# Performance work log

Hardware: AMD Instinct MI355X
Metric: run time of the kernel (lower is better)

## Reference

```python
import jax, jax.numpy as jnp
import numpy as np

N_NODES = 100000
N_EDGES = 1000000
F_IN = 128
HID = 128
OUT = 64


def setup_inputs() -> dict:
    key = jax.random.key(0)
    ks = jax.random.split(key, 8)
    node_features = jax.random.normal(ks[0], (N_NODES, F_IN), dtype=jnp.float32)
    edge_index = jax.random.randint(ks[1], (2, N_EDGES), 0, N_NODES, dtype=jnp.int64)
    s1 = 1.0 / np.sqrt(F_IN)
    s2 = 1.0 / np.sqrt(HID)
    W1 = jax.random.uniform(ks[2], (F_IN, HID), jnp.float32, -s1, s1)
    b1 = jax.random.uniform(ks[3], (HID,), jnp.float32, -s1, s1)
    W2 = jax.random.uniform(ks[4], (HID, HID), jnp.float32, -s2, s2)
    b2 = jax.random.uniform(ks[5], (HID,), jnp.float32, -s2, s2)
    Wp = jax.random.uniform(ks[6], (HID, OUT), jnp.float32, -s2, s2)
    bp = jax.random.uniform(ks[7], (OUT,), jnp.float32, -s2, s2)
    return {"node_features": node_features, "edge_index": edge_index,
            "W1": W1, "b1": b1, "W2": W2, "b2": b2, "Wp": Wp, "bp": bp}


def reference(node_features, edge_index, W1, b1, W2, b2, Wp, bp):
    # encoder: Linear -> ReLU -> Linear
    h = jax.nn.relu(node_features @ W1 + b1) @ W2 + b2  # [N, HID]
    src = edge_index[0]
    dst = edge_index[1]
    # per-edge gather of h[src], scatter-add into dst (segment reduce)
    messages = jax.ops.segment_sum(h[src], dst, num_segments=h.shape[0])  # [N, HID]
    h = h + messages
    pooled = jnp.mean(h, axis=0)  # [HID]
    return pooled @ Wp + bp  # [OUT]
```

## Files before the change

### kernel.cpp

```cpp
#include <hip/hip_runtime.h>
#include <hip/hip_bf16.h>
#include <stdint.h>

typedef __attribute__((ext_vector_type(8))) short short8;
typedef __attribute__((ext_vector_type(4))) float f32x4;
typedef __attribute__((ext_vector_type(4))) int i32x4;

#define RANGE  51200
#define RWORDS 25600
#define NSL    32
#define NFRAG  16

static __device__ __forceinline__ short to_bf16s(float f) {
  __hip_bfloat16 h = __float2bfloat16(f);
  return __builtin_bit_cast(short, h);
}

__global__ __launch_bounds__(1024) void k_histprep(
    const int* __restrict__ e, unsigned* __restrict__ priv,
    short* __restrict__ frag, const float* __restrict__ W1, int E) {
  __shared__ unsigned cnt[RWORDS];
  __shared__ int is64s;
  int b = blockIdx.x, tid = threadIdx.x;
  if (b < NFRAG) {
    int idx = b * 1024 + tid;
    int k = idx >> 7, col = idx & 127;
    int ct = col >> 4, ks = k >> 5, lh = (k >> 3) & 3, ee = k & 7;
    int lane = lh * 16 + (col & 15);
    frag[((ct * 4 + ks) * 64 + lane) * 8 + ee] = to_bf16s(W1[idx]);
    return;
  }
  int h = b - NFRAG;
  int r = h >> 5, s = h & (NSL - 1);
  if (tid < 64) {
    unsigned long long bl = __ballot(e[2 * tid + 1] == 0);
    if (tid == 0) is64s = (__popcll(bl) > 32) ? 1 : 0;
  }
  for (int j = tid; j < RWORDS; j += 1024) cnt[j] = 0u;
  __syncthreads();
  int is64 = is64s;
  unsigned base = (unsigned)r * RANGE;
  int nq = E >> 2;
  int qlo = (int)((long long)s * nq / NSL);
  int qhi = (int)((long long)(s + 1) * nq / NSL);
  for (int q = qlo + tid; q < qhi; q += 1024) {
    i32x4 v;
    if (is64) {
      i32x4 a = *reinterpret_cast<const i32x4*>(e + 8 * (size_t)q);
      i32x4 bb = *reinterpret_cast<const i32x4*>(e + 8 * (size_t)q + 4);
      v = i32x4{a[0], a[2], bb[0], bb[2]};
    } else {
      v = *reinterpret_cast<const i32x4*>(e + 4 * (size_t)q);
    }
#pragma unroll
    for (int k = 0; k < 4; ++k) {
      unsigned loc = (unsigned)v[k] - base;
      if (loc < (unsigned)RANGE)
        atomicAdd(&cnt[loc >> 1], 1u << (16 * (loc & 1)));
    }
  }
  if (s == 0) {
    int tail = E & 3;
    if (tid < tail) {
      int idx = E - tail + tid;
      unsigned loc = (unsigned)(is64 ? e[2 * idx] : e[idx]) - base;
      if (loc < (unsigned)RANGE)
        atomicAdd(&cnt[loc >> 1], 1u << (16 * (loc & 1)));
    }
  }
  __syncthreads();
  unsigned* dst = priv + (size_t)h * RWORDS;
  for (int j = tid; j < RWORDS; j += 1024) dst[j] = cnt[j];
}

__global__ __launch_bounds__(256) void k_main(
    const float* __restrict__ X, const short* __restrict__ w1frag,
    const float* __restrict__ b1, const unsigned* __restrict__ priv,
    const float* __restrict__ wdegG, float* __restrict__ partials,
    int nNodes) {
  __shared__ __align__(16) short w1s[16384];
  __shared__ __align__(16) short xs[8192];
  __shared__ __align__(16) float scratch[320];

  int tid = threadIdx.x;
  {
    const f32x4* src = reinterpret_cast<const f32x4*>(w1frag);
    f32x4* dst = reinterpret_cast<f32x4*>(w1s);
#pragma unroll
    for (int i = 0; i < 8; ++i) dst[tid + i * 256] = src[tid + i * 256];
  }
  unsigned* degacc = (unsigned*)scratch;
  float* wdeg_s = scratch + 256;

  int lane = tid & 63, wave = tid >> 6;
  int rA = lane & 15;
  int kh = lane >> 4;

  float b1r[8];
#pragma unroll
  for (int ct = 0; ct < 8; ++ct) b1r[ct] = b1[ct * 16 + rA];

  float sl[8] = {0, 0, 0, 0, 0, 0, 0, 0};
  int nChunks = (nNodes + 63) >> 6;
  __syncthreads();

  for (int c = blockIdx.x; c < nChunks; c += gridDim.x) {
    int row0 = c << 6;
#pragma unroll
    for (int p = 0; p < 4; ++p) {
      int j = p * 256 + tid;
      int rl = j >> 4, kc = j & 15;
      int grow = row0 + rl;
      if (grow > nNodes - 1) grow = nNodes - 1;
      const f32x4* gp =
          reinterpret_cast<const f32x4*>(X + (size_t)grow * 128 + kc * 8);
      f32x4 lo = gp[0], hi = gp[1];
      short8 v;
#pragma unroll
      for (int ee = 0; ee < 4; ++ee) {
        v[ee] = to_bf16s(lo[ee]);
        v[4 + ee] = to_bf16s(hi[ee]);
      }
      int u = rl * 16 + (kc ^ (rl & 7));
      *reinterpret_cast<short8*>(&xs[u * 8]) = v;
    }
    if (wdegG) {
      if (tid < 64) {
        int row = row0 + tid;
        wdeg_s[tid] = (row < nNodes) ? wdegG[row] : 0.f;
      }
    } else {
      int r = row0 / RANGE;
      int w0 = (row0 - r * RANGE) >> 1;
      int j = tid & 31, sg = tid >> 5;
      const unsigned* pp =
          priv + ((size_t)(r * NSL + sg * 4)) * RWORDS + w0 + j;
      unsigned ssum = 0;
#pragma unroll
      for (int q = 0; q < 4; ++q) ssum += pp[(size_t)q * RWORDS];
      degacc[sg * 32 + j] = ssum;
    }
    __syncthreads();
    if (!wdegG && tid < 32) {
      unsigned wsum = 0;
#pragma unroll
      for (int g = 0; g < 8; ++g) wsum += degacc[g * 32 + tid];
      wdeg_s[2 * tid] = 1.0f + (float)(wsum & 0xFFFFu);
      wdeg_s[2 * tid + 1] = 1.0f + (float)(wsum >> 16);
    }
    int rloc = wave * 16 + rA;
    f32x4 acc[8];
#pragma unroll
    for (int ct = 0; ct < 8; ++ct) acc[ct] = f32x4{0.f, 0.f, 0.f, 0.f};
#pragma unroll
    for (int ks = 0; ks < 4; ++ks) {
      int kc = ks * 4 + kh;
      int u = rloc * 16 + (kc ^ (rloc & 7));
      short8 a = *reinterpret_cast<const short8*>(&xs[u * 8]);
#pragma unroll
      for (int ct = 0; ct < 8; ++ct) {
        short8 bfr = *reinterpret_cast<const short8*>(
            &w1s[((ct * 4 + ks) * 64 + lane) * 8]);
        acc[ct] = __builtin_amdgcn_mfma_f32_16x16x32_bf16(a, bfr, acc[ct], 0, 0, 0);
      }
    }
    __syncthreads();
#pragma unroll
    for (int rr = 0; rr < 4; ++rr) {
      int rl = wave * 16 + kh * 4 + rr;
      float w = (row0 + rl < nNodes) ? wdeg_s[rl] : 0.0f;
#pragma unroll
      for (int ct = 0; ct < 8; ++ct)
        sl[ct] += w * fmaxf(acc[ct][rr] + b1r[ct], 0.f);
    }
    __syncthreads();
  }

  if (tid < 128) scratch[tid] = 0.f;
  __syncthreads();
#pragma unroll
  for (int ct = 0; ct < 8; ++ct) {
    float v = sl[ct];
    v += __shfl_xor(v, 16);
    v += __shfl_xor(v, 32);
    if (kh == 0) atomicAdd(&scratch[ct * 16 + rA], v);
  }
  __syncthreads();
  if (tid < 128) partials[(size_t)blockIdx.x * 128 + tid] = scratch[tid];
}

__global__ __launch_bounds__(1024) void k_final(
    const float* __restrict__ partials, int B, const float* __restrict__ W2,
    const float* __restrict__ b2, const float* __restrict__ Wp,
    const float* __restrict__ bp, float* __restrict__ out,
    float totalW, float invN) {
  __shared__ float accsA[32 * 128];
  __shared__ float sv[128];
  __shared__ float pooled[128];
  int t = threadIdx.x;
  {
    int cg = t & 31, slc = t >> 5;
    f32x4 s = f32x4{0.f, 0.f, 0.f, 0.f};
    for (int r = slc; r < B; r += 32)
      s += *reinterpret_cast<const f32x4*>(partials + (size_t)r * 128 + cg * 4);
    *reinterpret_cast<f32x4*>(&accsA[slc * 128 + cg * 4]) = s;
  }
  __syncthreads();
  if (t < 128) {
    float v = 0.f;
#pragma unroll
    for (int i = 0; i < 32; ++i) v += accsA[i * 128 + t];
    sv[t] = v;
  }
  __syncthreads();
  {
    int col = t & 127, sl8 = t >> 7;
    float a = 0.f;
#pragma unroll
    for (int kk = 0; kk < 16; ++kk) {
      int k = sl8 * 16 + kk;
      a += sv[k] * W2[k * 128 + col];
    }
    accsA[sl8 * 128 + col] = a;
  }
  __syncthreads();
  if (t < 128) {
    float v = totalW * b2[t];
#pragma unroll
    for (int i = 0; i < 8; ++i) v += accsA[i * 128 + t];
    pooled[t] = v * invN;
  }
  __syncthreads();
  if (t < 512) {
    int o = t & 63, s2 = t >> 6;
    float a = 0.f;
#pragma unroll
    for (int kk = 0; kk < 16; ++kk) {
      int k = s2 * 16 + kk;
      a += pooled[k] * Wp[k * 64 + o];
    }
    accsA[s2 * 64 + o] = a;
  }
  __syncthreads();
  if (t < 64) {
    float v = bp[t];
#pragma unroll
    for (int i = 0; i < 8; ++i) v += accsA[i * 64 + t];
    out[t] = v;
  }
}

__global__ void k_zero(unsigned* __restrict__ p, int n) {
  int i = blockIdx.x * 256 + threadIdx.x;
  if (i < n) p[i] = 0u;
}
__global__ __launch_bounds__(256) void k_hist_fb(const int* __restrict__ e,
                                                 unsigned* __restrict__ deg,
                                                 int E) {
  __shared__ int is64s;
  int tid = threadIdx.x;
  if (tid < 64) {
    unsigned long long bl = __ballot(e[2 * tid + 1] == 0);
    if (tid == 0) is64s = (__popcll(bl) > 32) ? 1 : 0;
  }
  __syncthreads();
  int is64 = is64s;
  int stride = gridDim.x * blockDim.x;
  for (int i = blockIdx.x * blockDim.x + tid; i < E; i += stride)
    atomicAdd(&deg[is64 ? (unsigned)e[2 * i] : (unsigned)e[i]], 1u);
}
__global__ void k_cvt(const unsigned* __restrict__ deg,
                      float* __restrict__ wdeg, int N) {
  int i = blockIdx.x * 256 + threadIdx.x;
  if (i < N) wdeg[i] = 1.0f + (float)deg[i];
}

extern "C" void kernel_launch(void* const* d_in, const int* in_sizes, int n_in,
                              void* d_out, int out_size, void* d_ws, size_t ws_size,
                              hipStream_t stream) {
  const float* X  = (const float*)d_in[0];
  const int*   ei = (const int*)d_in[1];
  const float* W1 = (const float*)d_in[2];
  const float* b1 = (const float*)d_in[3];
  const float* W2 = (const float*)d_in[4];
  const float* b2 = (const float*)d_in[5];
  const float* Wp = (const float*)d_in[6];
  const float* bp = (const float*)d_in[7];

  int N = in_sizes[0] / 128;
  int E = in_sizes[1] / 2;
  int nChunks = (N + 63) >> 6;
  int mb = nChunks < 521 ? nChunks : 521;

  size_t privB = (size_t)2 * NSL * RWORDS * 4;
  size_t fragB = (16384 * 2 + 255) & ~(size_t)255;
  size_t wdegB = ((size_t)N * 4 + 255) & ~(size_t)255;
  size_t partB = ((size_t)mb * 128 * 4 + 255) & ~(size_t)255;
  size_t fixed = privB + fragB + wdegB + partB + 512;

  bool fast = (N <= 2 * RANGE) && (E / NSL <= 60000) && (ws_size >= fixed);

  char* p = (char*)d_ws;
  unsigned* priv = (unsigned*)p;  p += privB;
  short* frag = (short*)p;        p += fragB;
  float* wdeg = (float*)p;        p += wdegB;
  float* parts = (float*)p;

  if (fast) {
    k_histprep<<<NFRAG + 2 * NSL, 1024, 0, stream>>>(ei, priv, frag, W1, E);
    k_main<<<mb, 256, 0, stream>>>(X, frag, b1, priv, (const float*)nullptr,
                                   parts, N);
  } else {
    k_histprep<<<NFRAG, 1024, 0, stream>>>(ei, priv, frag, W1, E);
    k_zero<<<(N + 255) / 256, 256, 0, stream>>>((unsigned*)wdeg, N);
    k_hist_fb<<<2048, 256, 0, stream>>>(ei, (unsigned*)wdeg, E);
    k_cvt<<<(N + 255) / 256, 256, 0, stream>>>((unsigned*)wdeg, wdeg, N);
    k_main<<<mb, 256, 0, stream>>>(X, frag, b1, priv, wdeg, parts, N);
  }
  k_final<<<1, 1024, 0, stream>>>(parts, mb, W2, b2, Wp, bp, (float*)d_out,
                                  (float)N + (float)E, 1.0f / (float)N);
}
```

Measured before the change: 39.15 us.

## Split degree merge into own kernel and make main loop per-wave without LDS staging

```diff
diff --git a/kernel.cpp b/kernel.cpp
--- a/kernel.cpp
+++ b/kernel.cpp
@@ -4,11 +4,12 @@
 
 typedef __attribute__((ext_vector_type(8))) short short8;
 typedef __attribute__((ext_vector_type(4))) float f32x4;
+typedef __attribute__((ext_vector_type(2))) float f32x2;
 typedef __attribute__((ext_vector_type(4))) int i32x4;
 
 #define RANGE  51200
 #define RWORDS 25600
-#define NSL    32
+#define NSL    64
 #define NFRAG  16
 
 static __device__ __forceinline__ short to_bf16s(float f) {
@@ -31,7 +32,7 @@
     return;
   }
   int h = b - NFRAG;
-  int r = h >> 5, s = h & (NSL - 1);
+  int r = h & 1, s = h >> 1;
   if (tid < 64) {
     unsigned long long bl = __ballot(e[2 * tid + 1] == 0);
     if (tid == 0) is64s = (__popcll(bl) > 32) ? 1 : 0;
@@ -73,14 +74,35 @@
   for (int j = tid; j < RWORDS; j += 1024) dst[j] = cnt[j];
 }
 
+__global__ __launch_bounds__(256) void k_merge(const unsigned* __restrict__ priv,
+                                               float* __restrict__ wdeg, int N) {
+  int g = blockIdx.x * 256 + threadIdx.x;
+  if (g >= 2 * RWORDS) return;
+  int r = (g >= RWORDS) ? 1 : 0;
+  int word = g - r * RWORDS;
+  const unsigned* p = priv + (size_t)r * RWORDS + word;
+  unsigned lo = 0, hi = 0;
+#pragma unroll 8
+  for (int s = 0; s < NSL; ++s) {
+    unsigned v = p[(size_t)(2 * s) * RWORDS];
+    lo += v & 0xFFFFu;
+    hi += v >> 16;
+  }
+  int n0 = r * RANGE + 2 * word;
+  if (n0 + 1 < N) {
+    *reinterpret_cast<f32x2*>(wdeg + n0) =
+        f32x2{1.0f + (float)lo, 1.0f + (float)hi};
+  } else if (n0 < N) {
+    wdeg[n0] = 1.0f + (float)lo;
+  }
+}
+
 __global__ __launch_bounds__(256) void k_main(
     const float* __restrict__ X, const short* __restrict__ w1frag,
-    const float* __restrict__ b1, const unsigned* __restrict__ priv,
-    const float* __restrict__ wdegG, float* __restrict__ partials,
-    int nNodes) {
+    const float* __restrict__ b1, const float* __restrict__ wdeg,
+    float* __restrict__ partials, int nNodes) {
   __shared__ __align__(16) short w1s[16384];
-  __shared__ __align__(16) short xs[8192];
-  __shared__ __align__(16) float scratch[320];
+  __shared__ float sred[128];
 
   int tid = threadIdx.x;
   {
@@ -89,8 +111,7 @@
 #pragma unroll
     for (int i = 0; i < 8; ++i) dst[tid + i * 256] = src[tid + i * 256];
   }
-  unsigned* degacc = (unsigned*)scratch;
-  float* wdeg_s = scratch + 256;
+  if (tid < 128) sred[tid] = 0.f;
 
   int lane = tid & 63, wave = tid >> 6;
   int rA = lane & 15;
@@ -101,62 +122,31 @@
   for (int ct = 0; ct < 8; ++ct) b1r[ct] = b1[ct * 16 + rA];
 
   float sl[8] = {0, 0, 0, 0, 0, 0, 0, 0};
-  int nChunks = (nNodes + 63) >> 6;
-  __syncthreads();
-
-  for (int c = blockIdx.x; c < nChunks; c += gridDim.x) {
-    int row0 = c << 6;
-#pragma unroll
-    for (int p = 0; p < 4; ++p) {
-      int j = p * 256 + tid;
-      int rl = j >> 4, kc = j & 15;
-      int grow = row0 + rl;
-      if (grow > nNodes - 1) grow = nNodes - 1;
-      const f32x4* gp =
-          reinterpret_cast<const f32x4*>(X + (size_t)grow * 128 + kc * 8);
-      f32x4 lo = gp[0], hi = gp[1];
-      short8 v;
+  int nChunks = (nNodes + 15) >> 4;
+  int gw = blockIdx.x * 4 + wave;
+  int nw = gridDim.x * 4;
+  __syncthreads();
+
+  for (int c = gw; c < nChunks; c += nw) {
+    int row0 = c << 4;
+    int rowA = row0 + rA;
+    if (rowA > nNodes - 1) rowA = nNodes - 1;
+    const float* xp = X + (size_t)rowA * 128 + kh * 8;
+
+    f32x4 acc[8];
+#pragma unroll
+    for (int ct = 0; ct < 8; ++ct) acc[ct] = f32x4{0.f, 0.f, 0.f, 0.f};
+
+#pragma unroll
+    for (int ks = 0; ks < 4; ++ks) {
+      f32x4 lo = *reinterpret_cast<const f32x4*>(xp + ks * 32);
+      f32x4 hi = *reinterpret_cast<const f32x4*>(xp + ks * 32 + 4);
+      short8 a;
 #pragma unroll
       for (int ee = 0; ee < 4; ++ee) {
-        v[ee] = to_bf16s(lo[ee]);
-        v[4 + ee] = to_bf16s(hi[ee]);
+        a[ee] = to_bf16s(lo[ee]);
+        a[4 + ee] = to_bf16s(hi[ee]);
       }
-      int u = rl * 16 + (kc ^ (rl & 7));
-      *reinterpret_cast<short8*>(&xs[u * 8]) = v;
-    }
-    if (wdegG) {
-      if (tid < 64) {
-        int row = row0 + tid;
-        wdeg_s[tid] = (row < nNodes) ? wdegG[row] : 0.f;
-      }
-    } else {
-      int r = row0 / RANGE;
-      int w0 = (row0 - r * RANGE) >> 1;
-      int j = tid & 31, sg = tid >> 5;
-      const unsigned* pp =
-          priv + ((size_t)(r * NSL + sg * 4)) * RWORDS + w0 + j;
-      unsigned ssum = 0;
-#pragma unroll
-      for (int q = 0; q < 4; ++q) ssum += pp[(size_t)q * RWORDS];
-      degacc[sg * 32 + j] = ssum;
-    }
-    __syncthreads();
-    if (!wdegG && tid < 32) {
-      unsigned wsum = 0;
-#pragma unroll
-      for (int g = 0; g < 8; ++g) wsum += degacc[g * 32 + tid];
-      wdeg_s[2 * tid] = 1.0f + (float)(wsum & 0xFFFFu);
-      wdeg_s[2 * tid + 1] = 1.0f + (float)(wsum >> 16);
-    }
-    int rloc = wave * 16 + rA;
-    f32x4 acc[8];
-#pragma unroll
-    for (int ct = 0; ct < 8; ++ct) acc[ct] = f32x4{0.f, 0.f, 0.f, 0.f};
-#pragma unroll
-    for (int ks = 0; ks < 4; ++ks) {
-      int kc = ks * 4 + kh;
-      int u = rloc * 16 + (kc ^ (rloc & 7));
-      short8 a = *reinterpret_cast<const short8*>(&xs[u * 8]);
 #pragma unroll
       for (int ct = 0; ct < 8; ++ct) {
         short8 bfr = *reinterpret_cast<const short8*>(
@@ -164,29 +154,26 @@
         acc[ct] = __builtin_amdgcn_mfma_f32_16x16x32_bf16(a, bfr, acc[ct], 0, 0, 0);
       }
     }
-    __syncthreads();
+
 #pragma unroll
     for (int rr = 0; rr < 4; ++rr) {
-      int rl = wave * 16 + kh * 4 + rr;
-      float w = (row0 + rl < nNodes) ? wdeg_s[rl] : 0.0f;
+      int row = row0 + kh * 4 + rr;
+      float w = (row < nNodes) ? wdeg[row] : 0.0f;
 #pragma unroll
       for (int ct = 0; ct < 8; ++ct)
         sl[ct] += w * fmaxf(acc[ct][rr] + b1r[ct], 0.f);
     }
-    __syncthreads();
-  }
-
-  if (tid < 128) scratch[tid] = 0.f;
-  __syncthreads();
+  }
+
 #pragma unroll
   for (int ct = 0; ct < 8; ++ct) {
     float v = sl[ct];
     v += __shfl_xor(v, 16);
     v += __shfl_xor(v, 32);
-    if (kh == 0) atomicAdd(&scratch[ct * 16 + rA], v);
-  }
-  __syncthreads();
-  if (tid < 128) partials[(size_t)blockIdx.x * 128 + tid] = scratch[tid];
+    if (kh == 0) atomicAdd(&sred[ct * 16 + rA], v);
+  }
+  __syncthreads();
+  if (tid < 128) partials[(size_t)blockIdx.x * 128 + tid] = sred[tid];
 }
 
 __global__ __launch_bounds__(1024) void k_final(
@@ -289,8 +276,10 @@
 
   int N = in_sizes[0] / 128;
   int E = in_sizes[1] / 2;
-  int nChunks = (N + 63) >> 6;
-  int mb = nChunks < 521 ? nChunks : 521;
+  int nChunks = (N + 15) >> 4;
+  int mb = 782;
+  if (nChunks < 2 * mb) mb = (nChunks + 7) / 8 * 2;
+  if (mb < 1) mb = 1;
 
   size_t privB = (size_t)2 * NSL * RWORDS * 4;
   size_t fragB = (16384 * 2 + 255) & ~(size_t)255;
@@ -308,15 +297,14 @@
 
   if (fast) {
     k_histprep<<<NFRAG + 2 * NSL, 1024, 0, stream>>>(ei, priv, frag, W1, E);
-    k_main<<<mb, 256, 0, stream>>>(X, frag, b1, priv, (const float*)nullptr,
-                                   parts, N);
+    k_merge<<<(2 * RWORDS + 255) / 256, 256, 0, stream>>>(priv, wdeg, N);
   } else {
     k_histprep<<<NFRAG, 1024, 0, stream>>>(ei, priv, frag, W1, E);
     k_zero<<<(N + 255) / 256, 256, 0, stream>>>((unsigned*)wdeg, N);
     k_hist_fb<<<2048, 256, 0, stream>>>(ei, (unsigned*)wdeg, E);
     k_cvt<<<(N + 255) / 256, 256, 0, stream>>>((unsigned*)wdeg, wdeg, N);
-    k_main<<<mb, 256, 0, stream>>>(X, frag, b1, priv, wdeg, parts, N);
-  }
+  }
+  k_main<<<mb, 256, 0, stream>>>(X, frag, b1, wdeg, parts, N);
   k_final<<<1, 1024, 0, stream>>>(parts, mb, W2, b2, Wp, bp, (float*)d_out,
                                   (float)N + (float)E, 1.0f / (float)N);
 }
```

After: 44.37 us. 13.3% more time.

## Split degree histogram into four ranges and merge in a dedicated kernel

Applied to the files above, without the earlier changes.

```diff
diff --git a/kernel.cpp b/kernel.cpp
--- a/kernel.cpp
+++ b/kernel.cpp
@@ -4,11 +4,13 @@
 
 typedef __attribute__((ext_vector_type(8))) short short8;
 typedef __attribute__((ext_vector_type(4))) float f32x4;
+typedef __attribute__((ext_vector_type(2))) float f32x2;
 typedef __attribute__((ext_vector_type(4))) int i32x4;
 
-#define RANGE  51200
-#define RWORDS 25600
-#define NSL    32
+#define NRANGE 4
+#define RNODES 25600
+#define RW     12800
+#define NS     32
 #define NFRAG  16
 
 static __device__ __forceinline__ short to_bf16s(float f) {
@@ -19,7 +21,7 @@
 __global__ __launch_bounds__(1024) void k_histprep(
     const int* __restrict__ e, unsigned* __restrict__ priv,
     short* __restrict__ frag, const float* __restrict__ W1, int E) {
-  __shared__ unsigned cnt[RWORDS];
+  __shared__ unsigned cnt[RW];
   __shared__ int is64s;
   int b = blockIdx.x, tid = threadIdx.x;
   if (b < NFRAG) {
@@ -31,18 +33,18 @@
     return;
   }
   int h = b - NFRAG;
-  int r = h >> 5, s = h & (NSL - 1);
+  int r = h / NS, s = h % NS;
   if (tid < 64) {
     unsigned long long bl = __ballot(e[2 * tid + 1] == 0);
     if (tid == 0) is64s = (__popcll(bl) > 32) ? 1 : 0;
   }
-  for (int j = tid; j < RWORDS; j += 1024) cnt[j] = 0u;
+  for (int j = tid; j < RW; j += 1024) cnt[j] = 0u;
   __syncthreads();
   int is64 = is64s;
-  unsigned base = (unsigned)r * RANGE;
+  unsigned base = (unsigned)r * RNODES;
   int nq = E >> 2;
-  int qlo = (int)((long long)s * nq / NSL);
-  int qhi = (int)((long long)(s + 1) * nq / NSL);
+  int qlo = (int)((long long)s * nq / NS);
+  int qhi = (int)((long long)(s + 1) * nq / NS);
   for (int q = qlo + tid; q < qhi; q += 1024) {
     i32x4 v;
     if (is64) {
@@ -55,7 +57,7 @@
 #pragma unroll
     for (int k = 0; k < 4; ++k) {
       unsigned loc = (unsigned)v[k] - base;
-      if (loc < (unsigned)RANGE)
+      if (loc < (unsigned)RNODES)
         atomicAdd(&cnt[loc >> 1], 1u << (16 * (loc & 1)));
     }
   }
@@ -64,23 +66,45 @@
     if (tid < tail) {
       int idx = E - tail + tid;
       unsigned loc = (unsigned)(is64 ? e[2 * idx] : e[idx]) - base;
-      if (loc < (unsigned)RANGE)
+      if (loc < (unsigned)RNODES)
         atomicAdd(&cnt[loc >> 1], 1u << (16 * (loc & 1)));
     }
   }
   __syncthreads();
-  unsigned* dst = priv + (size_t)h * RWORDS;
-  for (int j = tid; j < RWORDS; j += 1024) dst[j] = cnt[j];
+  unsigned* dst = priv + (size_t)h * RW;
+  for (int j = tid; j < RW; j += 1024) dst[j] = cnt[j];
+}
+
+__global__ __launch_bounds__(256) void k_merge(const unsigned* __restrict__ priv,
+                                               float* __restrict__ wdeg, int N) {
+  int g = blockIdx.x * 256 + threadIdx.x;
+  if (g >= NRANGE * RW) return;
+  int r = g / RW, word = g % RW;
+  const unsigned* p = priv + (size_t)(r * NS) * RW + word;
+  unsigned lo = 0, hi = 0;
+#pragma unroll 8
+  for (int s = 0; s < NS; ++s) {
+    unsigned v = p[(size_t)s * RW];
+    lo += v & 0xFFFFu;
+    hi += v >> 16;
+  }
+  int n0 = r * RNODES + 2 * word;
+  if (n0 + 1 < N) {
+    *reinterpret_cast<f32x2*>(wdeg + n0) =
+        f32x2{1.0f + (float)lo, 1.0f + (float)hi};
+  } else if (n0 < N) {
+    wdeg[n0] = 1.0f + (float)lo;
+  }
 }
 
 __global__ __launch_bounds__(256) void k_main(
     const float* __restrict__ X, const short* __restrict__ w1frag,
-    const float* __restrict__ b1, const unsigned* __restrict__ priv,
-    const float* __restrict__ wdegG, float* __restrict__ partials,
-    int nNodes) {
+    const float* __restrict__ b1, const float* __restrict__ wdeg,
+    float* __restrict__ partials, int nNodes) {
   __shared__ __align__(16) short w1s[16384];
   __shared__ __align__(16) short xs[8192];
-  __shared__ __align__(16) float scratch[320];
+  __shared__ float wdeg_s[64];
+  __shared__ float sred[128];
 
   int tid = threadIdx.x;
   {
@@ -89,8 +113,7 @@
 #pragma unroll
     for (int i = 0; i < 8; ++i) dst[tid + i * 256] = src[tid + i * 256];
   }
-  unsigned* degacc = (unsigned*)scratch;
-  float* wdeg_s = scratch + 256;
+  if (tid < 128) sred[tid] = 0.f;
 
   int lane = tid & 63, wave = tid >> 6;
   int rA = lane & 15;
@@ -124,30 +147,12 @@
       int u = rl * 16 + (kc ^ (rl & 7));
       *reinterpret_cast<short8*>(&xs[u * 8]) = v;
     }
-    if (wdegG) {
-      if (tid < 64) {
-        int row = row0 + tid;
-        wdeg_s[tid] = (row < nNodes) ? wdegG[row] : 0.f;
-      }
-    } else {
-      int r = row0 / RANGE;
-      int w0 = (row0 - r * RANGE) >> 1;
-      int j = tid & 31, sg = tid >> 5;
-      const unsigned* pp =
-          priv + ((size_t)(r * NSL + sg * 4)) * RWORDS + w0 + j;
-      unsigned ssum = 0;
-#pragma unroll
-      for (int q = 0; q < 4; ++q) ssum += pp[(size_t)q * RWORDS];
-      degacc[sg * 32 + j] = ssum;
+    if (tid < 64) {
+      int row = row0 + tid;
+      wdeg_s[tid] = (row < nNodes) ? wdeg[row] : 0.f;
     }
     __syncthreads();
-    if (!wdegG && tid < 32) {
-      unsigned wsum = 0;
-#pragma unroll
-      for (int g = 0; g < 8; ++g) wsum += degacc[g * 32 + tid];
-      wdeg_s[2 * tid] = 1.0f + (float)(wsum & 0xFFFFu);
-      wdeg_s[2 * tid + 1] = 1.0f + (float)(wsum >> 16);
-    }
+
     int rloc = wave * 16 + rA;
     f32x4 acc[8];
 #pragma unroll
@@ -164,11 +169,10 @@
         acc[ct] = __builtin_amdgcn_mfma_f32_16x16x32_bf16(a, bfr, acc[ct], 0, 0, 0);
       }
     }
-    __syncthreads();
 #pragma unroll
     for (int rr = 0; rr < 4; ++rr) {
       int rl = wave * 16 + kh * 4 + rr;
-      float w = (row0 + rl < nNodes) ? wdeg_s[rl] : 0.0f;
+      float w = wdeg_s[rl];
 #pragma unroll
       for (int ct = 0; ct < 8; ++ct)
         sl[ct] += w * fmaxf(acc[ct][rr] + b1r[ct], 0.f);
@@ -176,17 +180,15 @@
     __syncthreads();
   }
 
-  if (tid < 128) scratch[tid] = 0.f;
-  __syncthreads();
 #pragma unroll
   for (int ct = 0; ct < 8; ++ct) {
     float v = sl[ct];
     v += __shfl_xor(v, 16);
     v += __shfl_xor(v, 32);
-    if (kh == 0) atomicAdd(&scratch[ct * 16 + rA], v);
-  }
-  __syncthreads();
-  if (tid < 128) partials[(size_t)blockIdx.x * 128 + tid] = scratch[tid];
+    if (kh == 0) atomicAdd(&sred[ct * 16 + rA], v);
+  }
+  __syncthreads();
+  if (tid < 128) partials[(size_t)blockIdx.x * 128 + tid] = sred[tid];
 }
 
 __global__ __launch_bounds__(1024) void k_final(
@@ -201,6 +203,7 @@
   {
     int cg = t & 31, slc = t >> 5;
     f32x4 s = f32x4{0.f, 0.f, 0.f, 0.f};
+#pragma unroll 4
     for (int r = slc; r < B; r += 32)
       s += *reinterpret_cast<const f32x4*>(partials + (size_t)r * 128 + cg * 4);
     *reinterpret_cast<f32x4*>(&accsA[slc * 128 + cg * 4]) = s;
@@ -292,13 +295,13 @@
   int nChunks = (N + 63) >> 6;
   int mb = nChunks < 521 ? nChunks : 521;
 
-  size_t privB = (size_t)2 * NSL * RWORDS * 4;
+  size_t privB = (size_t)NRANGE * NS * RW * 4;
   size_t fragB = (16384 * 2 + 255) & ~(size_t)255;
   size_t wdegB = ((size_t)N * 4 + 255) & ~(size_t)255;
   size_t partB = ((size_t)mb * 128 * 4 + 255) & ~(size_t)255;
   size_t fixed = privB + fragB + wdegB + partB + 512;
 
-  bool fast = (N <= 2 * RANGE) && (E / NSL <= 60000) && (ws_size >= fixed);
+  bool fast = (N <= NRANGE * RNODES) && (E / NS <= 65000) && (ws_size >= fixed);
 
   char* p = (char*)d_ws;
   unsigned* priv = (unsigned*)p;  p += privB;
@@ -307,16 +310,15 @@
   float* parts = (float*)p;
 
   if (fast) {
-    k_histprep<<<NFRAG + 2 * NSL, 1024, 0, stream>>>(ei, priv, frag, W1, E);
-    k_main<<<mb, 256, 0, stream>>>(X, frag, b1, priv, (const float*)nullptr,
-                                   parts, N);
+    k_histprep<<<NFRAG + NRANGE * NS, 1024, 0, stream>>>(ei, priv, frag, W1, E);
+    k_merge<<<(NRANGE * RW + 255) / 256, 256, 0, stream>>>(priv, wdeg, N);
   } else {
     k_histprep<<<NFRAG, 1024, 0, stream>>>(ei, priv, frag, W1, E);
     k_zero<<<(N + 255) / 256, 256, 0, stream>>>((unsigned*)wdeg, N);
     k_hist_fb<<<2048, 256, 0, stream>>>(ei, (unsigned*)wdeg, E);
     k_cvt<<<(N + 255) / 256, 256, 0, stream>>>((unsigned*)wdeg, wdeg, N);
-    k_main<<<mb, 256, 0, stream>>>(X, frag, b1, priv, wdeg, parts, N);
-  }
+  }
+  k_main<<<mb, 256, 0, stream>>>(X, frag, b1, wdeg, parts, N);
   k_final<<<1, 1024, 0, stream>>>(parts, mb, W2, b2, Wp, bp, (float*)d_out,
                                   (float)N + (float)E, 1.0f / (float)N);
 }
```

New measurement: 37.02 us. 5.4% less time.
